# Kernel tuning notes

Measured on AMD Instinct MI355X. Metric: run time of the kernel, lower is better.

## Reference

```python
import jax, jax.numpy as jnp
import numpy as np
import math

B, L, D, H = 2, 2048, 1024, 16
HD = D // H  # head dim = 64


def setup_inputs() -> dict:
    key = jax.random.key(0)
    ks = jax.random.split(key, 5)
    s = 0.02
    return {
        "x": jax.random.normal(ks[0], (B, L, D), dtype=jnp.float32),
        "w_qkv": jax.random.normal(ks[1], (D, 3 * D), dtype=jnp.float32) * s,
        "b_qkv": jnp.zeros((3 * D,), dtype=jnp.float32),
        "w_out": jax.random.normal(ks[2], (D, D), dtype=jnp.float32) * s,
        "b_out": jnp.zeros((D,), dtype=jnp.float32),
    }


def reference(x, w_qkv, b_qkv, w_out, b_out):
    Bc, Lc, Dc = x.shape
    qkv = x @ w_qkv + b_qkv  # [B, L, 3D]
    q, k, v = jnp.split(qkv, 3, axis=-1)
    # [B, H, L, hd]
    q = q.reshape(Bc, Lc, H, HD).transpose(0, 2, 1, 3)
    k = k.reshape(Bc, Lc, H, HD).transpose(0, 2, 1, 3)
    v = v.reshape(Bc, Lc, H, HD).transpose(0, 2, 1, 3)
    scores = jnp.einsum("bhqd,bhkd->bhqk", q, k) / math.sqrt(HD)
    causal = jnp.tril(jnp.ones((Lc, Lc), dtype=bool))
    scores = jnp.where(causal[None, None, :, :], scores, -jnp.inf)
    probs = jax.nn.softmax(scores, axis=-1)
    outs = jnp.einsum("bhqk,bhkd->bhqd", probs, v)  # [B, H, L, hd]
    outs = outs.transpose(0, 2, 1, 3).reshape(Bc, Lc, Dc)
    return outs @ w_out + b_out
```

## Files before the change

### kernel.cpp

```cpp
#include <hip/hip_runtime.h>
#include <hip/hip_bf16.h>


using bf16x8 = __attribute__((ext_vector_type(8))) short;
using f32x4  = __attribute__((ext_vector_type(4))) float;

static __device__ __forceinline__ unsigned short f2b(float f) {
  unsigned u = __builtin_bit_cast(unsigned, f);
  unsigned r = (u + 0x7fffu + ((u >> 16) & 1u)) >> 16;
  return (unsigned short)r;
}

static __device__ __forceinline__ unsigned cvtpk(float lo, float hi) {
  unsigned r;
  asm("v_cvt_pk_bf16_f32 %0, %1, %2" : "=v"(r) : "v"(lo), "v"(hi));
  return r;
}

static __device__ __forceinline__ void gl_lds16(const void* g, void* l) {
  __builtin_amdgcn_global_load_lds(
      (const __attribute__((address_space(1))) unsigned int*)g,
      (__attribute__((address_space(3))) unsigned int*)l, 16, 0, 0);
}

__global__ __launch_bounds__(256) void convert_bf16(
    const float* __restrict__ in, unsigned short* __restrict__ out, int n8) {
  int i = blockIdx.x * 256 + threadIdx.x;
  if (i >= n8) return;
  const float4* p = reinterpret_cast<const float4*>(in) + (size_t)i * 2;
  float4 a = p[0], b = p[1];
  bf16x8 o;
  o[0] = f2b(a.x); o[1] = f2b(a.y); o[2] = f2b(a.z); o[3] = f2b(a.w);
  o[4] = f2b(b.x); o[5] = f2b(b.y); o[6] = f2b(b.z); o[7] = f2b(b.w);
  reinterpret_cast<bf16x8*>(out)[i] = o;
}

__global__ __launch_bounds__(256) void transpose_convert(
    const float* __restrict__ w, unsigned short* __restrict__ wt, int K, int N) {
  int idx = blockIdx.x * 256 + threadIdx.x;
  int n  = idx % N;
  int k0 = (idx / N) * 8;
  if (k0 >= K) return;
  bf16x8 o;
#pragma unroll
  for (int j = 0; j < 8; ++j) o[j] = f2b(w[(size_t)(k0 + j) * N + n]);
  *reinterpret_cast<bf16x8*>(&wt[(size_t)n * K + k0]) = o;
}

__global__ __launch_bounds__(256) void transpose_v(
    const unsigned short* __restrict__ vb, unsigned short* __restrict__ vt) {
  __shared__ unsigned short T[64][72];
  const int bh = blockIdx.y, l0 = blockIdx.x * 64;
  const int row = threadIdx.x >> 2;
  const int qc  = threadIdx.x & 3;
#pragma unroll
  for (int h = 0; h < 2; ++h) {
    bf16x8 v = *reinterpret_cast<const bf16x8*>(
        &vb[((size_t)bh * 2048 + l0 + row) * 64 + h * 32 + qc * 8]);
#pragma unroll
    for (int j = 0; j < 8; ++j) T[h * 32 + qc * 8 + j][row] = (unsigned short)v[j];
  }
  __syncthreads();
#pragma unroll
  for (int h = 0; h < 2; ++h) {
    bf16x8 o = *reinterpret_cast<const bf16x8*>(&T[row][h * 32 + qc * 8]);
    *reinterpret_cast<bf16x8*>(
        &vt[((size_t)bh * 64 + row) * 2048 + l0 + h * 32 + qc * 8]) = o;
  }
}

__global__ __launch_bounds__(512) void gemm_qkv(
    const unsigned short* __restrict__ A,
    const unsigned short* __restrict__ Bt,
    const float* __restrict__ bias,
    unsigned short* __restrict__ qb, unsigned short* __restrict__ kb,
    unsigned short* __restrict__ vb) {
  __shared__ __align__(16) unsigned short lA[256 * 64];
  __shared__ __align__(16) unsigned short lB[128 * 64];
  const int t = threadIdx.x;
  const int lin = blockIdx.y * 24 + blockIdx.x;
  const int nb  = (lin & 7) * 48 + (lin >> 3);
  const int bm = nb / 24, bn = nb % 24;
  const int s0 = (nb * 5) & 15;
  const int w = t >> 6, lane = t & 63;
  const int lr = lane & 15, lg = lane >> 4;
  const int wm = (w >> 1) * 64, wn = (w & 1) * 64;
  const int g8  = lane >> 3;
  const int swz = ((lane & 7) * 16) ^ (g8 << 4);

  f32x4 acc[4][4];
#pragma unroll
  for (int i = 0; i < 4; ++i)
#pragma unroll
    for (int j = 0; j < 4; ++j) acc[i][j] = f32x4{0.f, 0.f, 0.f, 0.f};

  const size_t am = (size_t)bm * 256, bnr = (size_t)bn * 128;

  for (int kt = 0; kt < 16; ++kt) {
    const int k0 = ((kt + s0) & 15) * 64;
#pragma unroll
    for (int i = 0; i < 4; ++i) {
      const int rs = i * 64 + w * 8;
      gl_lds16((const char*)(A + (am + rs + g8) * 1024 + k0) + swz,
               (char*)lA + rs * 128);
    }
#pragma unroll
    for (int i = 0; i < 2; ++i) {
      const int rs = i * 64 + w * 8;
      gl_lds16((const char*)(Bt + (bnr + rs + g8) * 1024 + k0) + swz,
               (char*)lB + rs * 128);
    }
    __syncthreads();
#pragma unroll
    for (int kk = 0; kk < 64; kk += 32) {
      bf16x8 af[4], bfr[4];
#pragma unroll
      for (int fm = 0; fm < 4; ++fm) {
        int row = wm + fm * 16 + lr;
        af[fm] = *reinterpret_cast<const bf16x8*>(
            (const char*)lA + row * 128 + ((2 * kk + lg * 16) ^ ((lr & 7) << 4)));
      }
#pragma unroll
      for (int fn = 0; fn < 4; ++fn) {
        int row = wn + fn * 16 + lr;
        bfr[fn] = *reinterpret_cast<const bf16x8*>(
            (const char*)lB + row * 128 + ((2 * kk + lg * 16) ^ ((lr & 7) << 4)));
      }
#pragma unroll
      for (int fm = 0; fm < 4; ++fm)
#pragma unroll
        for (int fn = 0; fn < 4; ++fn)
          acc[fm][fn] = __builtin_amdgcn_mfma_f32_16x16x32_bf16(
              af[fm], bfr[fn], acc[fm][fn], 0, 0, 0);
    }
    __syncthreads();
  }

#pragma unroll
  for (int fm = 0; fm < 4; ++fm) {
#pragma unroll
    for (int fn = 0; fn < 4; ++fn) {
#pragma unroll
      for (int r = 0; r < 4; ++r) {
        int row = bm * 256 + wm + fm * 16 + lg * 4 + r;
        int col = bn * 128 + wn + fn * 16 + lr;
        float v = acc[fm][fn][r] + bias[col];
        int bb = row >> 11, l = row & 2047;
        int which = col >> 10, hn = col & 1023;
        int h = hn >> 6, d = hn & 63;
        int bh = bb * 16 + h;
        if (which == 0)
          qb[((size_t)bh * 2048 + l) * 64 + d] = f2b(v * 0.180336879f);
        else if (which == 1)
          kb[((size_t)bh * 2048 + l) * 64 + d] = f2b(v);
        else
          vb[((size_t)bh * 2048 + l) * 64 + d] = f2b(v);
      }
    }
  }
}

__global__ __launch_bounds__(256) void gemm_out(
    const unsigned short* __restrict__ A,
    const unsigned short* __restrict__ Bt,
    const float* __restrict__ bias, float* __restrict__ outf) {
  __shared__ __align__(16) unsigned short lA[128 * 64];
  __shared__ __align__(16) unsigned short lB[64 * 64];
  const int t = threadIdx.x;
  const int lin = blockIdx.y * 16 + blockIdx.x;
  const int nb  = (lin & 7) * 64 + (lin >> 3);
  const int bm = nb >> 4, bn = nb & 15;
  const int s0 = (nb * 5) & 15;
  const int w = t >> 6, lane = t & 63;
  const int lr = lane & 15, lg = lane >> 4;
  const int wm = (w >> 1) * 64, wn = (w & 1) * 32;
  const int g8  = lane >> 3;
  const int swz = ((lane & 7) * 16) ^ (g8 << 4);

  f32x4 acc[4][2];
#pragma unroll
  for (int i = 0; i < 4; ++i)
#pragma unroll
    for (int j = 0; j < 2; ++j) acc[i][j] = f32x4{0.f, 0.f, 0.f, 0.f};

  const size_t am = (size_t)bm * 128, bnr = (size_t)bn * 64;

  for (int kt = 0; kt < 16; ++kt) {
    const int k0 = ((kt + s0) & 15) * 64;
#pragma unroll
    for (int i = 0; i < 4; ++i) {
      const int rs = i * 32 + w * 8;
      gl_lds16((const char*)(A + (am + rs + g8) * 1024 + k0) + swz,
               (char*)lA + rs * 128);
    }
#pragma unroll
    for (int i = 0; i < 2; ++i) {
      const int rs = i * 32 + w * 8;
      gl_lds16((const char*)(Bt + (bnr + rs + g8) * 1024 + k0) + swz,
               (char*)lB + rs * 128);
    }
    __syncthreads();
#pragma unroll
    for (int kk = 0; kk < 64; kk += 32) {
      bf16x8 af[4], bfr[2];
#pragma unroll
      for (int fm = 0; fm < 4; ++fm) {
        int row = wm + fm * 16 + lr;
        af[fm] = *reinterpret_cast<const bf16x8*>(
            (const char*)lA + row * 128 + ((2 * kk + lg * 16) ^ ((lr & 7) << 4)));
      }
#pragma unroll
      for (int fn = 0; fn < 2; ++fn) {
        int row = wn + fn * 16 + lr;
        bfr[fn] = *reinterpret_cast<const bf16x8*>(
            (const char*)lB + row * 128 + ((2 * kk + lg * 16) ^ ((lr & 7) << 4)));
      }
#pragma unroll
      for (int fm = 0; fm < 4; ++fm)
#pragma unroll
        for (int fn = 0; fn < 2; ++fn)
          acc[fm][fn] = __builtin_amdgcn_mfma_f32_16x16x32_bf16(
              af[fm], bfr[fn], acc[fm][fn], 0, 0, 0);
    }
    __syncthreads();
  }

#pragma unroll
  for (int fm = 0; fm < 4; ++fm)
#pragma unroll
    for (int fn = 0; fn < 2; ++fn)
#pragma unroll
      for (int r = 0; r < 4; ++r) {
        int row = bm * 128 + wm + fm * 16 + lg * 4 + r;
        int col = bn * 64 + wn + fn * 16 + lr;
        outf[(size_t)row * 1024 + col] = acc[fm][fn][r] + bias[col];
      }
}

__global__ __launch_bounds__(256, 2) void attn_kernel(
    const unsigned short* __restrict__ qb, const unsigned short* __restrict__ kb,
    const unsigned short* __restrict__ vt, unsigned short* __restrict__ attnb) {
  __shared__ __align__(16) unsigned short lK[2][128 * 64];
  __shared__ __align__(16) unsigned short lV[2][2][64 * 64];
  __shared__ __align__(16) unsigned short pl[4][16 * 128];
  const int bid = blockIdx.x;
  const int xcd = bid & 7, pos = bid >> 3;
  const int half = pos >> 5, idx = pos & 31;
  const int bh = xcd * 4 + half * 2 + (idx >> 4);
  const int qt = half ? (15 - (idx & 15)) : (idx & 15);
  const int q0 = qt * 128;
  const int w = threadIdx.x >> 6, lane = threadIdx.x & 63;
  const int lr = lane & 15, lg = lane >> 4;
  const int g8  = lane >> 3;
  const int swz = ((lane & 7) * 16) ^ (g8 << 4);

  const unsigned short* Kg = kb + (size_t)bh * 2048 * 64;
  const unsigned short* Vg = vt + (size_t)bh * 64 * 2048;

  auto stage = [&](int buf, int c) {
    const size_t kv0 = (size_t)c * 128;
#pragma unroll
    for (int i = 0; i < 4; ++i) {
      const int rs = i * 32 + w * 8;
      gl_lds16((const char*)(Kg + (kv0 + rs + g8) * 64) + swz,
               (char*)&lK[buf][0] + rs * 128);
    }
#pragma unroll
    for (int h = 0; h < 2; ++h)
#pragma unroll
      for (int i = 0; i < 2; ++i) {
        const int rs = i * 32 + w * 8;
        gl_lds16((const char*)(Vg + (size_t)(rs + g8) * 2048 + kv0 + h * 64) + swz,
                 (char*)&lV[buf][h][0] + rs * 128);
      }
  };

  bf16x8 qf[2][2];
#pragma unroll
  for (int qi = 0; qi < 2; ++qi)
#pragma unroll
    for (int kk = 0; kk < 2; ++kk)
      qf[qi][kk] = *reinterpret_cast<const bf16x8*>(
          &qb[((size_t)bh * 2048 + q0 + w * 32 + qi * 16 + lr) * 64 + kk * 32 + lg * 8]);

  f32x4 acc[2][4];
#pragma unroll
  for (int qi = 0; qi < 2; ++qi)
#pragma unroll
    for (int i = 0; i < 4; ++i) acc[qi][i] = f32x4{0.f, 0.f, 0.f, 0.f};
  float m[2] = {-1e30f, -1e30f}, rs[2] = {0.f, 0.f};

  const int nc = qt + 1;
  stage(0, 0);

  for (int c = 0; c < nc; ++c) {
    const int cur = c & 1;
    __syncthreads();
    if (c + 1 < nc) stage(cur ^ 1, c + 1);

    f32x4 s[2][8];
#pragma unroll
    for (int qi = 0; qi < 2; ++qi)
#pragma unroll
      for (int i = 0; i < 8; ++i) s[qi][i] = f32x4{0.f, 0.f, 0.f, 0.f};
#pragma unroll
    for (int nf = 0; nf < 8; ++nf) {
      const int row = nf * 16 + lr;
      bf16x8 k0 = *reinterpret_cast<const bf16x8*>(
          (const char*)&lK[cur][0] + row * 128 + ((lg * 16) ^ ((lr & 7) << 4)));
      bf16x8 k1 = *reinterpret_cast<const bf16x8*>(
          (const char*)&lK[cur][0] + row * 128 + ((64 + lg * 16) ^ ((lr & 7) << 4)));
#pragma unroll
      for (int qi = 0; qi < 2; ++qi) {
        s[qi][nf] = __builtin_amdgcn_mfma_f32_16x16x32_bf16(k0, qf[qi][0], s[qi][nf], 0, 0, 0);
        s[qi][nf] = __builtin_amdgcn_mfma_f32_16x16x32_bf16(k1, qf[qi][1], s[qi][nf], 0, 0, 0);
      }
    }

#pragma unroll
    for (int qi = 0; qi < 2; ++qi) {
      const int qrow = q0 + w * 32 + qi * 16 + lr;
      const bool diag = (c * 128 + 127) > (q0 + w * 32 + qi * 16);
      float ps[8][4];
      float mx = -1e30f;
      if (diag) {
#pragma unroll
        for (int nf = 0; nf < 8; ++nf)
#pragma unroll
          for (int r = 0; r < 4; ++r) {
            int key = c * 128 + nf * 16 + lg * 4 + r;
            float sv = (key <= qrow) ? s[qi][nf][r] : -1e30f;
            ps[nf][r] = sv;
            mx = fmaxf(mx, sv);
          }
      } else {
#pragma unroll
        for (int nf = 0; nf < 8; ++nf)
#pragma unroll
          for (int r = 0; r < 4; ++r) {
            ps[nf][r] = s[qi][nf][r];
            mx = fmaxf(mx, ps[nf][r]);
          }
      }
      mx = fmaxf(mx, __shfl_xor(mx, 16));
      mx = fmaxf(mx, __shfl_xor(mx, 32));
      if (__any(mx > m[qi] + 8.f)) {
        float mn = fmaxf(m[qi], mx);
        float scl = exp2f(m[qi] - mn);
        m[qi] = mn;
        rs[qi] *= scl;
#pragma unroll
        for (int df = 0; df < 4; ++df) acc[qi][df] *= scl;
      }
      float ss = 0.f;
#pragma unroll
      for (int nf = 0; nf < 8; ++nf)
#pragma unroll
        for (int r = 0; r < 4; ++r) {
          float pe = exp2f(ps[nf][r] - m[qi]);
          ps[nf][r] = pe;
          ss += pe;
        }
      ss += __shfl_xor(ss, 16);
      ss += __shfl_xor(ss, 32);
      rs[qi] += ss;

#pragma unroll
      for (int nf = 0; nf < 8; ++nf) {
        uint2 pk;
        pk.x = cvtpk(ps[nf][0], ps[nf][1]);
        pk.y = cvtpk(ps[nf][2], ps[nf][3]);
        *reinterpret_cast<uint2*>(
            (char*)&pl[w][0] + lr * 256 + ((nf * 32 + lg * 8) ^ ((lr & 7) << 4))) = pk;
      }
#pragma unroll
      for (int kk = 0; kk < 4; ++kk) {
        bf16x8 pf = *reinterpret_cast<const bf16x8*>(
            (const char*)&pl[w][0] + lr * 256 + ((kk * 64 + lg * 16) ^ ((lr & 7) << 4)));
#pragma unroll
        for (int df = 0; df < 4; ++df) {
          const int row = df * 16 + lr;
          bf16x8 vf = *reinterpret_cast<const bf16x8*>(
              (const char*)&lV[cur][kk >> 1][0] + row * 128 +
              (((kk & 1) * 64 + lg * 16) ^ ((lr & 7) << 4)));
          acc[qi][df] = __builtin_amdgcn_mfma_f32_16x16x32_bf16(vf, pf, acc[qi][df], 0, 0, 0);
        }
      }
    }
  }

  const int b = bh >> 4, h = bh & 15;
#pragma unroll
  for (int qi = 0; qi < 2; ++qi) {
    float inv = 1.f / rs[qi];
    int qrow = q0 + w * 32 + qi * 16 + lr;
#pragma unroll
    for (int df = 0; df < 4; ++df) {
      ushort4 ov;
      ov.x = f2b(acc[qi][df][0] * inv); ov.y = f2b(acc[qi][df][1] * inv);
      ov.z = f2b(acc[qi][df][2] * inv); ov.w = f2b(acc[qi][df][3] * inv);
      *reinterpret_cast<ushort4*>(
          &attnb[((size_t)b * 2048 + qrow) * 1024 + h * 64 + df * 16 + lg * 4]) = ov;
    }
  }
}

extern "C" void kernel_launch(void* const* d_in, const int* in_sizes, int n_in,
                              void* d_out, int out_size, void* d_ws, size_t ws_size,
                              hipStream_t stream) {
  const float* x     = (const float*)d_in[0];
  const float* w_qkv = (const float*)d_in[1];
  const float* b_qkv = (const float*)d_in[2];
  const float* w_out = (const float*)d_in[3];
  const float* b_out = (const float*)d_in[4];
  float* out = (float*)d_out;
  char* ws = (char*)d_ws;

  unsigned short* xb    = (unsigned short*)(ws);
  unsigned short* vt    = (unsigned short*)(ws);
  unsigned short* wqkvt = (unsigned short*)(ws + 8388608);
  unsigned short* woutt = (unsigned short*)(ws + 14680064);
  unsigned short* qb    = (unsigned short*)(ws + 16777216);
  unsigned short* kb    = (unsigned short*)(ws + 25165824);
  unsigned short* vb    = (unsigned short*)(ws + 33554432);
  unsigned short* attnb = (unsigned short*)(ws + 41943040);

  convert_bf16<<<2048, 256, 0, stream>>>(x, xb, 4194304 / 8);
  transpose_convert<<<1536, 256, 0, stream>>>(w_qkv, wqkvt, 1024, 3072);
  transpose_convert<<<512, 256, 0, stream>>>(w_out, woutt, 1024, 1024);
  gemm_qkv<<<dim3(24, 16), 512, 0, stream>>>(xb, wqkvt, b_qkv, qb, kb, vb);
  transpose_v<<<dim3(32, 32), 256, 0, stream>>>(vb, vt);
  attn_kernel<<<512, 256, 0, stream>>>(qb, kb, vt, attnb);
  gemm_out<<<dim3(16, 32), 256, 0, stream>>>(attnb, woutt, b_out, out);
}
```

Measured before the change: 130.9 us.

## Merge input conversion kernels and tree-reduce softmax max/sum in attention

Folds the three fp32-to-bf16 conversion and transpose kernels into a single launch that dispatches on block index, removing two kernel launches and their gaps. In the attention kernel, the row max and row sum are now computed with a shallow tree of fmax and adds instead of serial chains, which shortens dependency latency. Softmax for both query sub-tiles now finishes before any P tile is packed and multiplied, so ps becomes a [2][8][4] array and register pressure rises.

Measured after the change: 133.5 us. 2.0% more time.

```diff
diff --git a/kernel.cpp b/kernel.cpp
--- a/kernel.cpp
+++ b/kernel.cpp
@@ -23,28 +23,38 @@
       (__attribute__((address_space(3))) unsigned int*)l, 16, 0, 0);
 }
 
-__global__ __launch_bounds__(256) void convert_bf16(
-    const float* __restrict__ in, unsigned short* __restrict__ out, int n8) {
-  int i = blockIdx.x * 256 + threadIdx.x;
-  if (i >= n8) return;
-  const float4* p = reinterpret_cast<const float4*>(in) + (size_t)i * 2;
-  float4 a = p[0], b = p[1];
-  bf16x8 o;
-  o[0] = f2b(a.x); o[1] = f2b(a.y); o[2] = f2b(a.z); o[3] = f2b(a.w);
-  o[4] = f2b(b.x); o[5] = f2b(b.y); o[6] = f2b(b.z); o[7] = f2b(b.w);
-  reinterpret_cast<bf16x8*>(out)[i] = o;
-}
-
-__global__ __launch_bounds__(256) void transpose_convert(
-    const float* __restrict__ w, unsigned short* __restrict__ wt, int K, int N) {
-  int idx = blockIdx.x * 256 + threadIdx.x;
-  int n  = idx % N;
-  int k0 = (idx / N) * 8;
-  if (k0 >= K) return;
-  bf16x8 o;
-#pragma unroll
-  for (int j = 0; j < 8; ++j) o[j] = f2b(w[(size_t)(k0 + j) * N + n]);
-  *reinterpret_cast<bf16x8*>(&wt[(size_t)n * K + k0]) = o;
+__global__ __launch_bounds__(256) void prep_inputs(
+    const float* __restrict__ x, const float* __restrict__ w_qkv,
+    const float* __restrict__ w_out, unsigned short* __restrict__ xb,
+    unsigned short* __restrict__ wqkvt, unsigned short* __restrict__ woutt) {
+  const int bid = blockIdx.x, t = threadIdx.x;
+  if (bid < 2048) {
+    int i = bid * 256 + t;
+    const float4* p = reinterpret_cast<const float4*>(x) + (size_t)i * 2;
+    float4 a = p[0], b = p[1];
+    bf16x8 o;
+    o[0] = f2b(a.x); o[1] = f2b(a.y); o[2] = f2b(a.z); o[3] = f2b(a.w);
+    o[4] = f2b(b.x); o[5] = f2b(b.y); o[6] = f2b(b.z); o[7] = f2b(b.w);
+    reinterpret_cast<bf16x8*>(xb)[i] = o;
+  } else if (bid < 3584) {
+    int idx = (bid - 2048) * 256 + t;
+    int n = idx % 3072, k0 = (idx / 3072) * 8;
+    if (k0 < 1024) {
+      bf16x8 o;
+#pragma unroll
+      for (int j = 0; j < 8; ++j) o[j] = f2b(w_qkv[(size_t)(k0 + j) * 3072 + n]);
+      *reinterpret_cast<bf16x8*>(&wqkvt[(size_t)n * 1024 + k0]) = o;
+    }
+  } else {
+    int idx = (bid - 3584) * 256 + t;
+    int n = idx % 1024, k0 = (idx / 1024) * 8;
+    if (k0 < 1024) {
+      bf16x8 o;
+#pragma unroll
+      for (int j = 0; j < 8; ++j) o[j] = f2b(w_out[(size_t)(k0 + j) * 1024 + n]);
+      *reinterpret_cast<bf16x8*>(&woutt[(size_t)n * 1024 + k0]) = o;
+    }
+  }
 }
 
 __global__ __launch_bounds__(256) void transpose_v(
@@ -317,31 +327,29 @@
       }
     }
 
+    float ps[2][8][4];
 #pragma unroll
     for (int qi = 0; qi < 2; ++qi) {
       const int qrow = q0 + w * 32 + qi * 16 + lr;
       const bool diag = (c * 128 + 127) > (q0 + w * 32 + qi * 16);
-      float ps[8][4];
-      float mx = -1e30f;
-      if (diag) {
-#pragma unroll
-        for (int nf = 0; nf < 8; ++nf)
-#pragma unroll
-          for (int r = 0; r < 4; ++r) {
+      float g4[8];
+#pragma unroll
+      for (int nf = 0; nf < 8; ++nf) {
+#pragma unroll
+        for (int r = 0; r < 4; ++r) {
+          float sv = s[qi][nf][r];
+          if (diag) {
             int key = c * 128 + nf * 16 + lg * 4 + r;
-            float sv = (key <= qrow) ? s[qi][nf][r] : -1e30f;
-            ps[nf][r] = sv;
-            mx = fmaxf(mx, sv);
+            sv = (key <= qrow) ? sv : -1e30f;
           }
-      } else {
-#pragma unroll
-        for (int nf = 0; nf < 8; ++nf)
-#pragma unroll
-          for (int r = 0; r < 4; ++r) {
-            ps[nf][r] = s[qi][nf][r];
-            mx = fmaxf(mx, ps[nf][r]);
-          }
-      }
+          ps[qi][nf][r] = sv;
+        }
+        g4[nf] = fmaxf(fmaxf(ps[qi][nf][0], ps[qi][nf][1]),
+                       fmaxf(ps[qi][nf][2], ps[qi][nf][3]));
+      }
+      float a0 = fmaxf(g4[0], g4[1]), a1 = fmaxf(g4[2], g4[3]);
+      float a2 = fmaxf(g4[4], g4[5]), a3 = fmaxf(g4[6], g4[7]);
+      float mx = fmaxf(fmaxf(a0, a1), fmaxf(a2, a3));
       mx = fmaxf(mx, __shfl_xor(mx, 16));
       mx = fmaxf(mx, __shfl_xor(mx, 32));
       if (__any(mx > m[qi] + 8.f)) {
@@ -352,24 +360,29 @@
 #pragma unroll
         for (int df = 0; df < 4; ++df) acc[qi][df] *= scl;
       }
-      float ss = 0.f;
-#pragma unroll
-      for (int nf = 0; nf < 8; ++nf)
-#pragma unroll
-        for (int r = 0; r < 4; ++r) {
-          float pe = exp2f(ps[nf][r] - m[qi]);
-          ps[nf][r] = pe;
-          ss += pe;
-        }
+      float s4[8];
+#pragma unroll
+      for (int nf = 0; nf < 8; ++nf) {
+#pragma unroll
+        for (int r = 0; r < 4; ++r)
+          ps[qi][nf][r] = exp2f(ps[qi][nf][r] - m[qi]);
+        s4[nf] = (ps[qi][nf][0] + ps[qi][nf][1]) + (ps[qi][nf][2] + ps[qi][nf][3]);
+      }
+      float b0 = s4[0] + s4[1], b1 = s4[2] + s4[3];
+      float b2 = s4[4] + s4[5], b3 = s4[6] + s4[7];
+      float ss = (b0 + b1) + (b2 + b3);
       ss += __shfl_xor(ss, 16);
       ss += __shfl_xor(ss, 32);
       rs[qi] += ss;
-
+    }
+
+#pragma unroll
+    for (int qi = 0; qi < 2; ++qi) {
 #pragma unroll
       for (int nf = 0; nf < 8; ++nf) {
         uint2 pk;
-        pk.x = cvtpk(ps[nf][0], ps[nf][1]);
-        pk.y = cvtpk(ps[nf][2], ps[nf][3]);
+        pk.x = cvtpk(ps[qi][nf][0], ps[qi][nf][1]);
+        pk.y = cvtpk(ps[qi][nf][2], ps[qi][nf][3]);
         *reinterpret_cast<uint2*>(
             (char*)&pl[w][0] + lr * 256 + ((nf * 32 + lg * 8) ^ ((lr & 7) << 4))) = pk;
       }
@@ -425,9 +438,7 @@
   unsigned short* vb    = (unsigned short*)(ws + 33554432);
   unsigned short* attnb = (unsigned short*)(ws + 41943040);
 
-  convert_bf16<<<2048, 256, 0, stream>>>(x, xb, 4194304 / 8);
-  transpose_convert<<<1536, 256, 0, stream>>>(w_qkv, wqkvt, 1024, 3072);
-  transpose_convert<<<512, 256, 0, stream>>>(w_out, woutt, 1024, 1024);
+  prep_inputs<<<4096, 256, 0, stream>>>(x, w_qkv, w_out, xb, wqkvt, woutt);
   gemm_qkv<<<dim3(24, 16), 512, 0, stream>>>(xb, wqkvt, b_qkv, qb, kb, vb);
   transpose_v<<<dim3(32, 32), 256, 0, stream>>>(vb, vt);
   attn_kernel<<<512, 256, 0, stream>>>(qb, kb, vt, attnb);
```
